# Performance work log

Measured on AMD Instinct MI355X. Metric: run time of the kernel, lower is better.

The kernel has to match this reference:

```python
import jax, jax.numpy as jnp
import numpy as np

HEADS = 8
NEG = -1e9
EPS = 1e-9


def setup_inputs() -> dict:
    key = jax.random.key(0)
    ks = jax.random.split(key, 24)
    N, D, E = 2048, 512, 64
    s = 0.02
    inp = {
        "xyz": jax.random.normal(ks[0], (N, 3), jnp.float32),
        "str_feat": jax.random.normal(ks[1], (N, D), jnp.float32),
        "esm_feat": jax.random.normal(ks[2], (N, E), jnp.float32),
        "y_hat": jax.random.uniform(ks[3], (N, 1), jnp.float32),
        "distance_mask": jax.random.randint(ks[4], (N, N), 0, 2, jnp.int32),
        "t": jnp.ones((1,), jnp.float32),
        "band_width": jnp.ones((1,), jnp.float32),
        "max_iter": 5,
        # main projections (torch Linear layout: y = x @ W.T + b)
        "Wq": jax.random.normal(ks[5], (D, D), jnp.float32) * s,
        "bq": jnp.zeros((D,), jnp.float32),
        "Wk": jax.random.normal(ks[6], (D, D), jnp.float32) * s,
        "bk": jnp.zeros((D,), jnp.float32),
        "Wv": jax.random.normal(ks[7], (D, D), jnp.float32) * s,
        "bv": jnp.zeros((D,), jnp.float32),
        "Wo": jax.random.normal(ks[8], (D, D), jnp.float32) * s,
        "bo": jnp.zeros((D,), jnp.float32),
        # esm projections (computed in the original forward but unused downstream)
        "Weq": jax.random.normal(ks[9], (E, E), jnp.float32) * s,
        "beq": jnp.zeros((E,), jnp.float32),
        "Wek": jax.random.normal(ks[10], (E, E), jnp.float32) * s,
        "bek": jnp.zeros((E,), jnp.float32),
        "Wev": jax.random.normal(ks[11], (E, E), jnp.float32) * s,
        "bev": jnp.zeros((E,), jnp.float32),
        "Weo": jax.random.normal(ks[12], (E, E), jnp.float32) * s,
        "beo": jnp.zeros((E,), jnp.float32),
    }
    return inp


def reference(xyz, str_feat, esm_feat, y_hat, distance_mask, t, band_width, max_iter,
              Wq, bq, Wk, bk, Wv, bv, Wo, bo,
              Weq, beq, Wek, bek, Wev, bev, Weo, beo):
    N, D = str_feat.shape
    h = HEADS
    dh = D // h

    q = str_feat @ Wq.T + bq
    k = str_feat @ Wk.T + bk
    v = str_feat @ Wv.T + bv
    # esm projections: computed in the original forward but never used (dead code; DCE'd under jit)
    _esm_q = esm_feat @ Weq.T + beq
    _esm_k = esm_feat @ Wek.T + bek
    _esm_v = esm_feat @ Wev.T + bev

    # [h, N, dh]
    qh = q.reshape(N, h, dh).transpose(1, 0, 2)
    kh = k.reshape(N, h, dh).transpose(1, 0, 2)
    vh = v.reshape(N, h, dh).transpose(1, 0, 2)

    scores = jnp.einsum('hnd,hmd->hnm', qh, kh) / jnp.sqrt(jnp.asarray(dh, qh.dtype))
    mask = (distance_mask > 0)[None]              # [1, N, N]
    yw = y_hat[:, 0][None, :]                     # [1, N] per-target weight
    inv_two_bw2 = 1.0 / (2.0 * band_width[0] ** 2)
    temp = t[0]

    def step(carry, _):
        xyz_c, _x = carry
        # squared pairwise distances via the expanded form (avoids [N,N,3])
        sq = jnp.sum(xyz_c * xyz_c, axis=-1)
        d2 = sq[:, None] + sq[None, :] - 2.0 * (xyz_c @ xyz_c.T)
        kern = jnp.exp(-d2 * inv_two_bw2)          # [N, N] band-width kernel
        logits = scores / temp + jnp.log(kern * yw + EPS)[None]
        logits = jnp.where(mask, logits, NEG)
        attn = jax.nn.softmax(logits, axis=-1)     # [h, N, N]
        xyz_new = jnp.einsum('nm,md->nd', attn.mean(0), xyz_c)  # mean-shift step
        x_new = jnp.einsum('hnm,hmd->hnd', attn, vh)            # [h, N, dh]
        return (xyz_new, x_new), None

    (xyz_out, xh), _ = jax.lax.scan(step, (xyz, jnp.zeros_like(vh)), None, length=max_iter)
    x = xh.transpose(1, 0, 2).reshape(N, D)
    out = x @ Wo.T + bo
    return xyz_out, out
```

## Files before the change

### kernel.cpp

```cpp
#include <hip/hip_runtime.h>


typedef __attribute__((ext_vector_type(8))) short bf16x8;
typedef __attribute__((ext_vector_type(4))) float f32x4;

__device__ __forceinline__ unsigned short f2bf(float f) {
    unsigned int u = __float_as_uint(f);
    u += 0x7fff + ((u >> 16) & 1);
    return (unsigned short)(u >> 16);
}
__device__ __forceinline__ float bf2f(unsigned short u) {
    return __uint_as_float((unsigned int)u << 16);
}

union EU { bf16x8 v; unsigned short u[8]; };

__global__ __launch_bounds__(256)
void conv_all(const float* __restrict__ strf,
              const float* __restrict__ Wq, const float* __restrict__ Wk,
              const float* __restrict__ Wv, const float* __restrict__ Wo,
              const int* __restrict__ dmask,
              unsigned short* __restrict__ sA, unsigned short* __restrict__ sW,
              unsigned char* __restrict__ mby)
{
    const long base = (long)(blockIdx.x * 256 + threadIdx.x) * 8;
    if (base >= 2097152) {
        const long rel = base - 2097152;
        int4 a = *reinterpret_cast<const int4*>(dmask + rel);
        int4 b = *reinterpret_cast<const int4*>(dmask + rel + 4);
        unsigned long long p = 0;
        p |= (a.x > 0) ? 0x01ULL : 0;  p |= (a.y > 0) ? 0x0100ULL : 0;
        p |= (a.z > 0) ? 0x010000ULL : 0;  p |= (a.w > 0) ? 0x01000000ULL : 0;
        p |= (b.x > 0) ? 0x0100000000ULL : 0;  p |= (b.y > 0) ? 0x010000000000ULL : 0;
        p |= (b.z > 0) ? 0x01000000000000ULL : 0;  p |= (b.w > 0) ? 0x0100000000000000ULL : 0;
        *reinterpret_cast<unsigned long long*>(mby + rel) = p;
        return;
    }
    const float* src;
    unsigned short* dst;
    if (base < 1048576) {
        src = strf + base; dst = sA + base;
    } else {
        const long rel = base - 1048576;
        const int seg = (int)(rel >> 18);
        const long off = rel & 262143;
        const float* Ws[4] = {Wq, Wk, Wv, Wo};
        src = Ws[seg] + off;
        dst = sW + (long)seg * 262144 + off;
    }
    float4 a = *reinterpret_cast<const float4*>(src);
    float4 b = *reinterpret_cast<const float4*>(src + 4);
    EU o;
    o.u[0] = f2bf(a.x); o.u[1] = f2bf(a.y); o.u[2] = f2bf(a.z); o.u[3] = f2bf(a.w);
    o.u[4] = f2bf(b.x); o.u[5] = f2bf(b.y); o.u[6] = f2bf(b.z); o.u[7] = f2bf(b.w);
    *reinterpret_cast<bf16x8*>(dst) = o.v;
}

__global__ __launch_bounds__(256)
void qkv_mfma(const unsigned short* __restrict__ sA,
              const unsigned short* __restrict__ sW,
              const float* __restrict__ bq, const float* __restrict__ bk,
              const float* __restrict__ bv,
              unsigned short* __restrict__ qh, unsigned short* __restrict__ kh,
              unsigned short* __restrict__ vT)
{
    const int z  = blockIdx.z;
    const int bx = blockIdx.x;
    const int by = blockIdx.y;
    const int tid = threadIdx.x;
    const int wv = tid >> 6;
    const int lane = tid & 63;
    const int row  = lane & 15;
    const int koct = (lane >> 4) * 8;
    const int n0 = bx * 64;

    const unsigned short* Ap = sA + (long)(n0 + wv * 16 + row) * 512;
    const unsigned short* Bp = sW + (long)z * 262144 + (long)(by * 64 + row) * 512;

    f32x4 acc[4] = {};
#pragma unroll
    for (int k0 = 0; k0 < 512; k0 += 32) {
        bf16x8 a = *reinterpret_cast<const bf16x8*>(Ap + k0 + koct);
#pragma unroll
        for (int t = 0; t < 4; t++) {
            bf16x8 b = *reinterpret_cast<const bf16x8*>(Bp + (long)(t * 16) * 512 + k0 + koct);
            acc[t] = __builtin_amdgcn_mfma_f32_16x16x32_bf16(a, b, acc[t], 0, 0, 0);
        }
    }

    if (z == 2) {
        const int rbase = n0 + wv * 16 + (lane >> 4) * 4;
#pragma unroll
        for (int t = 0; t < 4; t++) {
            const int d = by * 64 + t * 16 + (lane & 15);
            const float bb = bv[d];
            ushort4 o;
            o.x = f2bf(acc[t][0] + bb); o.y = f2bf(acc[t][1] + bb);
            o.z = f2bf(acc[t][2] + bb); o.w = f2bf(acc[t][3] + bb);
            *reinterpret_cast<ushort4*>(vT + (long)d * 2048 + rbase) = o;
        }
        return;
    }

    __shared__ float ls[64][68];
    const int lrb = wv * 16 + (lane >> 4) * 4;
    const int lcb = lane & 15;
#pragma unroll
    for (int t = 0; t < 4; t++)
#pragma unroll
        for (int r = 0; r < 4; r++)
            ls[lrb + r][t * 16 + lcb] = acc[t][r];
    __syncthreads();

    const float* bias = (z == 0) ? bq : bk;
    unsigned short* dst = (z == 0) ? qh : kh;
    const int r2 = tid >> 2;
    const int c2 = (tid & 3) * 16;
    float sv[16];
#pragma unroll
    for (int j = 0; j < 4; j++) {
        float4 s = *reinterpret_cast<const float4*>(&ls[r2][c2 + j * 4]);
        float4 bb = *reinterpret_cast<const float4*>(bias + by * 64 + c2 + j * 4);
        sv[j*4+0] = s.x + bb.x; sv[j*4+1] = s.y + bb.y;
        sv[j*4+2] = s.z + bb.z; sv[j*4+3] = s.w + bb.w;
    }
    EU o0, o1;
#pragma unroll
    for (int j = 0; j < 8; j++) { o0.u[j] = f2bf(sv[j]); o1.u[j] = f2bf(sv[8 + j]); }
    unsigned short* dp = dst + (long)(n0 + r2) * 512 + by * 64 + c2;
    *reinterpret_cast<bf16x8*>(dp)     = o0.v;
    *reinterpret_cast<bf16x8*>(dp + 8) = o1.v;
}

__global__ __launch_bounds__(256)
void scores_rows(const unsigned short* __restrict__ qh,
                 const unsigned short* __restrict__ kh,
                 const unsigned char* __restrict__ mby,
                 const float* __restrict__ tptr,
                 unsigned short* __restrict__ Ebf)
{
    const int h  = blockIdx.y;
    const int n0 = blockIdx.x * 16;
    const int tid = threadIdx.x;
    const int wv = tid >> 6;
    const int lane = tid & 63;
    const float scale = 1.0f / (8.0f * tptr[0]);

    __shared__ unsigned short lsb[4][16][260];

    const int arow = lane & 15;
    const int koct = (lane >> 4) * 8;
    const unsigned short* Aq = qh + (long)(n0 + arow) * 512 + h * 64;
    const bf16x8 aq0 = *reinterpret_cast<const bf16x8*>(Aq + koct);
    const bf16x8 aq1 = *reinterpret_cast<const bf16x8*>(Aq + 32 + koct);

    const int lr = (lane >> 4) * 4;
    const int lc = lane & 15;
    const int rlo = lane >> 5;
    const int cch = lane & 31;

#pragma unroll
    for (int half = 0; half < 2; half++) {
        const int mbase = wv * 512 + half * 256;
#pragma unroll
        for (int mt = 0; mt < 16; mt++) {
            const unsigned short* Bk = kh + (long)(mbase + mt * 16 + arow) * 512 + h * 64;
            bf16x8 b0 = *reinterpret_cast<const bf16x8*>(Bk + koct);
            bf16x8 b1 = *reinterpret_cast<const bf16x8*>(Bk + 32 + koct);
            f32x4 c = {};
            c = __builtin_amdgcn_mfma_f32_16x16x32_bf16(aq0, b0, c, 0, 0, 0);
            c = __builtin_amdgcn_mfma_f32_16x16x32_bf16(aq1, b1, c, 0, 0, 0);
#pragma unroll
            for (int r = 0; r < 4; r++)
                lsb[wv][lr + r][mt * 16 + lc] = f2bf(__expf(c[r] * scale));
        }
#pragma unroll
        for (int rp = 0; rp < 8; rp++) {
            const int row = rp * 2 + rlo;
            const int gn = n0 + row;
            const int m = mbase + cch * 8;
            EU e;
            e.v = *reinterpret_cast<const bf16x8*>(&lsb[wv][row][cch * 8]);
            unsigned long long mk =
                *reinterpret_cast<const unsigned long long*>(mby + (long)gn * 2048 + m);
            EU o;
#pragma unroll
            for (int j = 0; j < 8; j++)
                o.u[j] = ((mk >> (8 * j)) & 0xff) ? e.u[j] : (unsigned short)0;
            *reinterpret_cast<bf16x8*>(Ebf + ((long)h * 2048 + gn) * 2048 + m) = o.v;
        }
    }
}

__global__ __launch_bounds__(256)
void ms_iter(const unsigned short* __restrict__ Ebf,
             const float* __restrict__ xyz_src,
             float* __restrict__ xyz_dst,
             const float* __restrict__ y_hat,
             const float* __restrict__ bwp,
             unsigned short* __restrict__ gbf,
             float* __restrict__ invzb,
             int wlast)
{
    const int n = blockIdx.x;
    const int tid = threadIdx.x;
    const int lane = tid & 63;
    const int wave = tid >> 6;
    const int m0 = tid * 8;

    __shared__ unsigned short Es[8][4][512];
    __shared__ float red[64];

    {
        const unsigned short* gp = Ebf + (long)n * 2048 + wave * 512 + lane * 8;
#pragma unroll
        for (int h = 0; h < 8; h++) {
            __builtin_amdgcn_global_load_lds(
                (const __attribute__((address_space(1))) unsigned int*)(gp + (long)h * 4194304),
                (__attribute__((address_space(3))) unsigned int*)&Es[h][wave][0],
                16, 0, 0);
        }
    }

    const float bw = bwp[0];
    const float c2k = 1.0f / (2.0f * bw * bw);
    const float xn = xyz_src[n * 3 + 0];
    const float yn = xyz_src[n * 3 + 1];
    const float zn = xyz_src[n * 3 + 2];
    const float sqn = xn * xn + yn * yn + zn * zn;

    float mx[8], my[8], mz[8];
    {
        const float4* xp = reinterpret_cast<const float4*>(xyz_src + (long)m0 * 3);
        float4 a = xp[0], b = xp[1], c = xp[2], d = xp[3], e = xp[4], f = xp[5];
        mx[0]=a.x; my[0]=a.y; mz[0]=a.z;  mx[1]=a.w; my[1]=b.x; mz[1]=b.y;
        mx[2]=b.z; my[2]=b.w; mz[2]=c.x;  mx[3]=c.y; my[3]=c.z; mz[3]=c.w;
        mx[4]=d.x; my[4]=d.y; mz[4]=d.z;  mx[5]=d.w; my[5]=e.x; mz[5]=e.y;
        mx[6]=e.z; my[6]=e.w; mz[6]=f.x;  mx[7]=f.y; my[7]=f.z; mz[7]=f.w;
    }
    float4 yh0 = *reinterpret_cast<const float4*>(y_hat + m0);
    float4 yh1 = *reinterpret_cast<const float4*>(y_hat + m0 + 4);
    float yh[8] = {yh0.x, yh0.y, yh0.z, yh0.w, yh1.x, yh1.y, yh1.z, yh1.w};

    float g[8];
#pragma unroll
    for (int j = 0; j < 8; j++) {
        const float d2 = sqn + (mx[j]*mx[j] + my[j]*my[j] + mz[j]*mz[j])
                       - 2.0f * (xn*mx[j] + yn*my[j] + zn*mz[j]);
        g[j] = __expf(-d2 * c2k) * yh[j] + 1e-9f;
    }

    __syncthreads();

    EU E[8];
#pragma unroll
    for (int h = 0; h < 8; h++)
        E[h].v = *reinterpret_cast<const bf16x8*>(&Es[h][wave][lane * 8]);

    float z[8];
#pragma unroll
    for (int h = 0; h < 8; h++) {
        float zz = 0.f;
#pragma unroll
        for (int j = 0; j < 8; j++) zz += bf2f(E[h].u[j]) * g[j];
        z[h] = zz;
    }

#pragma unroll
    for (int h = 0; h < 8; h++) {
        float v = z[h];
#pragma unroll
        for (int off = 32; off > 0; off >>= 1) v += __shfl_down(v, off, 64);
        if (lane == 0) red[wave * 8 + h] = v;
    }
    __syncthreads();
    if (tid < 8) {
        const float s = red[tid] + red[8 + tid] + red[16 + tid] + red[24 + tid];
        const float iz = 1.0f / s;
        red[32 + tid] = iz;
        if (wlast) invzb[tid * 2048 + n] = iz;
    }
    __syncthreads();
    float invz[8];
#pragma unroll
    for (int h = 0; h < 8; h++) invz[h] = red[32 + h];

    float ax = 0.f, ay = 0.f, az = 0.f;
#pragma unroll
    for (int j = 0; j < 8; j++) {
        float w = 0.f;
#pragma unroll
        for (int h = 0; h < 8; h++) w += bf2f(E[h].u[j]) * invz[h];
        w *= 0.125f * g[j];
        ax += w * mx[j]; ay += w * my[j]; az += w * mz[j];
    }
    if (wlast) {
        EU og;
#pragma unroll
        for (int j = 0; j < 8; j++) og.u[j] = f2bf(g[j]);
        *reinterpret_cast<bf16x8*>(gbf + (long)n * 2048 + m0) = og.v;
    }

    float v3[3] = {ax, ay, az};
#pragma unroll
    for (int c = 0; c < 3; c++) {
        float v = v3[c];
#pragma unroll
        for (int off = 32; off > 0; off >>= 1) v += __shfl_down(v, off, 64);
        if (lane == 0) red[40 + c * 4 + wave] = v;
    }
    __syncthreads();
    if (tid < 3) {
        xyz_dst[n * 3 + tid] = red[40 + tid * 4 + 0] + red[40 + tid * 4 + 1] +
                               red[40 + tid * 4 + 2] + red[40 + tid * 4 + 3];
    }
}

__global__ __launch_bounds__(256)
void av_mfma(const unsigned short* __restrict__ Ebf,
             const unsigned short* __restrict__ gbf,
             const unsigned short* __restrict__ vT,
             float* __restrict__ P)
{
    const int h  = blockIdx.z;
    const int s  = blockIdx.y;
    const int bx = blockIdx.x;
    const int tid = threadIdx.x;
    const int wv = tid >> 6;
    const int lane = tid & 63;
    const int n0 = bx * 64;
    const int kc = s * 512;

    __shared__ unsigned short As[64][132];

    const int mrow = lane & 15;
    const int koct = (lane >> 4) * 8;
    const int srow = tid >> 4;
    const int skk  = (tid & 15) * 8;

    f32x4 acc[4] = {};
    for (int kt = 0; kt < 4; kt++) {
        const int kb = kc + kt * 128;
        __syncthreads();
#pragma unroll
        for (int l = 0; l < 4; l++) {
            const int row = l * 16 + srow;
            EU e, gg;
            e.v  = *reinterpret_cast<const bf16x8*>(Ebf + ((long)h * 2048 + n0 + row) * 2048 + kb + skk);
            gg.v = *reinterpret_cast<const bf16x8*>(gbf + (long)(n0 + row) * 2048 + kb + skk);
            EU a;
#pragma unroll
            for (int j = 0; j < 8; j++)
                a.u[j] = f2bf(bf2f(e.u[j]) * bf2f(gg.u[j]));
            *reinterpret_cast<bf16x8*>(&As[row][skk]) = a.v;
        }
        __syncthreads();
#pragma unroll
        for (int k2 = 0; k2 < 128; k2 += 32) {
            bf16x8 a = *reinterpret_cast<const bf16x8*>(&As[wv * 16 + mrow][k2 + koct]);
#pragma unroll
            for (int t = 0; t < 4; t++) {
                bf16x8 b = *reinterpret_cast<const bf16x8*>(
                    vT + ((long)h * 64 + t * 16 + mrow) * 2048 + kb + k2 + koct);
                acc[t] = __builtin_amdgcn_mfma_f32_16x16x32_bf16(a, b, acc[t], 0, 0, 0);
            }
        }
    }

    float* Pp = P + (long)s * 1048576;
    const int rbase = n0 + wv * 16 + (lane >> 4) * 4;
    const int dcol = lane & 15;
#pragma unroll
    for (int t = 0; t < 4; t++)
#pragma unroll
        for (int r = 0; r < 4; r++)
            Pp[(long)(rbase + r) * 512 + h * 64 + t * 16 + dcol] = acc[t][r];
}

__global__ __launch_bounds__(256)
void av_red(const float* __restrict__ P, const float* __restrict__ invzb,
            unsigned short* __restrict__ xc)
{
    const long idx = (long)(blockIdx.x * 256 + threadIdx.x) * 8;
    const int n = (int)(idx >> 9);
    const int d0 = (int)(idx & 511);
    const float iz = invzb[(d0 >> 6) * 2048 + n];
    float s[8] = {};
#pragma unroll
    for (int p = 0; p < 4; p++) {
        const float* pp = P + (long)p * 1048576 + idx;
        float4 a = *reinterpret_cast<const float4*>(pp);
        float4 b = *reinterpret_cast<const float4*>(pp + 4);
        s[0] += a.x; s[1] += a.y; s[2] += a.z; s[3] += a.w;
        s[4] += b.x; s[5] += b.y; s[6] += b.z; s[7] += b.w;
    }
    EU o;
#pragma unroll
    for (int j = 0; j < 8; j++) o.u[j] = f2bf(s[j] * iz);
    *reinterpret_cast<bf16x8*>(xc + idx) = o.v;
}

__global__ __launch_bounds__(256)
void out_mfma(const unsigned short* __restrict__ xc,
              const unsigned short* __restrict__ sW,
              const float* __restrict__ bo,
              float* __restrict__ out)
{
    const int bx = blockIdx.x;
    const int by = blockIdx.y;
    const int wv = threadIdx.x >> 6;
    const int lane = threadIdx.x & 63;
    const int row  = lane & 15;
    const int koct = (lane >> 4) * 8;
    const int n0 = bx * 64;

    const unsigned short* Ap = xc + (long)(n0 + wv * 16 + row) * 512;
    const unsigned short* Bp = sW + 3L * 262144 + (long)(by * 64 + row) * 512;

    f32x4 acc[4] = {};
#pragma unroll
    for (int k0 = 0; k0 < 512; k0 += 32) {
        bf16x8 a = *reinterpret_cast<const bf16x8*>(Ap + k0 + koct);
#pragma unroll
        for (int t = 0; t < 4; t++) {
            bf16x8 b = *reinterpret_cast<const bf16x8*>(Bp + (long)(t * 16) * 512 + k0 + koct);
            acc[t] = __builtin_amdgcn_mfma_f32_16x16x32_bf16(a, b, acc[t], 0, 0, 0);
        }
    }

    const int rbase = n0 + wv * 16 + (lane >> 4) * 4;
    const int dcol = lane & 15;
#pragma unroll
    for (int t = 0; t < 4; t++) {
        const int col = by * 64 + t * 16 + dcol;
        const float bb = bo[col];
#pragma unroll
        for (int r = 0; r < 4; r++)
            out[(long)(rbase + r) * 512 + col] = acc[t][r] + bb;
    }
}

extern "C" void kernel_launch(void* const* d_in, const int* in_sizes, int n_in,
                              void* d_out, int out_size, void* d_ws, size_t ws_size,
                              hipStream_t stream)
{
    (void)in_sizes; (void)n_in; (void)out_size; (void)ws_size;

    const float* xyz   = (const float*)d_in[0];
    const float* strf  = (const float*)d_in[1];
    const float* yhat  = (const float*)d_in[3];
    const int*   dmask = (const int*)d_in[4];
    const float* tptr  = (const float*)d_in[5];
    const float* bwptr = (const float*)d_in[6];
    const float* Wq = (const float*)d_in[8];
    const float* bq = (const float*)d_in[9];
    const float* Wk = (const float*)d_in[10];
    const float* bk = (const float*)d_in[11];
    const float* Wv = (const float*)d_in[12];
    const float* bv = (const float*)d_in[13];
    const float* Wo = (const float*)d_in[14];
    const float* bo = (const float*)d_in[15];
    float* outp = (float*)d_out;

    char* wsb = (char*)d_ws;
    float* Ppart         = (float*)(wsb);
    unsigned short* xc   = (unsigned short*)(wsb + (16L << 20));
    unsigned short* sA   = (unsigned short*)(wsb + (18L << 20));
    unsigned short* sW   = (unsigned short*)(wsb + (20L << 20));
    unsigned short* qh   = (unsigned short*)(wsb + (22L << 20));
    unsigned short* kh   = (unsigned short*)(wsb + (24L << 20));
    unsigned short* vT   = (unsigned short*)(wsb + (26L << 20));
    float* xyzA          = (float*)(wsb + (28L << 20));
    float* xyzB          = xyzA + 8192;
    unsigned char* mby   = (unsigned char*)(wsb + (30L << 20));
    unsigned short* Ebf  = (unsigned short*)(wsb + (34L << 20));
    unsigned short* gbf  = (unsigned short*)(wsb + (98L << 20));
    float* invzb         = (float*)(wsb + (106L << 20));

    dim3 blk(256, 1, 1);

    conv_all<<<dim3(3072), blk, 0, stream>>>(strf, Wq, Wk, Wv, Wo, dmask, sA, sW, mby);
    qkv_mfma<<<dim3(32, 8, 3), blk, 0, stream>>>(sA, sW, bq, bk, bv, qh, kh, vT);

    scores_rows<<<dim3(128, 8), blk, 0, stream>>>(qh, kh, mby, tptr, Ebf);

    const float* src = xyz;
    float* dsts[5] = {xyzA, xyzB, xyzA, xyzB, outp};
    for (int it = 0; it < 5; it++) {
        ms_iter<<<dim3(2048), blk, 0, stream>>>(Ebf, src, dsts[it], yhat, bwptr,
                                                gbf, invzb, it == 4 ? 1 : 0);
        src = dsts[it];
    }

    av_mfma<<<dim3(32, 4, 8), blk, 0, stream>>>(Ebf, gbf, vT, Ppart);
    av_red<<<dim3(512), blk, 0, stream>>>(Ppart, invzb, xc);
    out_mfma<<<dim3(32, 8), blk, 0, stream>>>(xc, sW, bo, outp + 6144);
}
```

Measured before the change: 318.6 us.

## Store masked scores row-major across heads and fuse split-K reduction into output GEMM

The masked exp-scores buffer moves from a head-major [h][n][m] layout to a row-major [n][h][m] layout. Each ms_iter block, which handles one row across all 8 heads, now reads one contiguous 32 KB region instead of 8 strided slices. The separate av_red kernel is removed: out_mfma now sums the four split-K partials, applies the normalizer and converts to bf16 inline. This saves a launch and an intermediate buffer round trip, but out_mfma now re-reads the fp32 partials once per output column block (8 times).

```diff
diff --git a/kernel.cpp b/kernel.cpp
--- a/kernel.cpp
+++ b/kernel.cpp
@@ -137,7 +137,7 @@
                  const unsigned short* __restrict__ kh,
                  const unsigned char* __restrict__ mby,
                  const float* __restrict__ tptr,
-                 unsigned short* __restrict__ Ebf)
+                 unsigned short* __restrict__ E2)
 {
     const int h  = blockIdx.y;
     const int n0 = blockIdx.x * 16;
@@ -187,13 +187,13 @@
 #pragma unroll
             for (int j = 0; j < 8; j++)
                 o.u[j] = ((mk >> (8 * j)) & 0xff) ? e.u[j] : (unsigned short)0;
-            *reinterpret_cast<bf16x8*>(Ebf + ((long)h * 2048 + gn) * 2048 + m) = o.v;
-        }
-    }
-}
-
-__global__ __launch_bounds__(256)
-void ms_iter(const unsigned short* __restrict__ Ebf,
+            *reinterpret_cast<bf16x8*>(E2 + (long)gn * 16384 + h * 2048 + m) = o.v;
+        }
+    }
+}
+
+__global__ __launch_bounds__(256)
+void ms_iter(const unsigned short* __restrict__ E2,
              const float* __restrict__ xyz_src,
              float* __restrict__ xyz_dst,
              const float* __restrict__ y_hat,
@@ -208,16 +208,16 @@
     const int wave = tid >> 6;
     const int m0 = tid * 8;
 
-    __shared__ unsigned short Es[8][4][512];
+    __shared__ unsigned short Es[16384];
     __shared__ float red[64];
 
     {
-        const unsigned short* gp = Ebf + (long)n * 2048 + wave * 512 + lane * 8;
-#pragma unroll
-        for (int h = 0; h < 8; h++) {
+        const unsigned short* gp = E2 + (long)n * 16384 + wave * 4096 + lane * 8;
+#pragma unroll
+        for (int c = 0; c < 8; c++) {
             __builtin_amdgcn_global_load_lds(
-                (const __attribute__((address_space(1))) unsigned int*)(gp + (long)h * 4194304),
-                (__attribute__((address_space(3))) unsigned int*)&Es[h][wave][0],
+                (const __attribute__((address_space(1))) unsigned int*)(gp + c * 512),
+                (__attribute__((address_space(3))) unsigned int*)&Es[wave * 4096 + c * 512],
                 16, 0, 0);
         }
     }
@@ -255,7 +255,7 @@
     EU E[8];
 #pragma unroll
     for (int h = 0; h < 8; h++)
-        E[h].v = *reinterpret_cast<const bf16x8*>(&Es[h][wave][lane * 8]);
+        E[h].v = *reinterpret_cast<const bf16x8*>(&Es[h * 2048 + m0]);
 
     float z[8];
 #pragma unroll
@@ -317,7 +317,7 @@
 }
 
 __global__ __launch_bounds__(256)
-void av_mfma(const unsigned short* __restrict__ Ebf,
+void av_mfma(const unsigned short* __restrict__ E2,
              const unsigned short* __restrict__ gbf,
              const unsigned short* __restrict__ vT,
              float* __restrict__ P)
@@ -346,7 +346,7 @@
         for (int l = 0; l < 4; l++) {
             const int row = l * 16 + srow;
             EU e, gg;
-            e.v  = *reinterpret_cast<const bf16x8*>(Ebf + ((long)h * 2048 + n0 + row) * 2048 + kb + skk);
+            e.v  = *reinterpret_cast<const bf16x8*>(E2 + (long)(n0 + row) * 16384 + h * 2048 + kb + skk);
             gg.v = *reinterpret_cast<const bf16x8*>(gbf + (long)(n0 + row) * 2048 + kb + skk);
             EU a;
 #pragma unroll
@@ -378,30 +378,8 @@
 }
 
 __global__ __launch_bounds__(256)
-void av_red(const float* __restrict__ P, const float* __restrict__ invzb,
-            unsigned short* __restrict__ xc)
-{
-    const long idx = (long)(blockIdx.x * 256 + threadIdx.x) * 8;
-    const int n = (int)(idx >> 9);
-    const int d0 = (int)(idx & 511);
-    const float iz = invzb[(d0 >> 6) * 2048 + n];
-    float s[8] = {};
-#pragma unroll
-    for (int p = 0; p < 4; p++) {
-        const float* pp = P + (long)p * 1048576 + idx;
-        float4 a = *reinterpret_cast<const float4*>(pp);
-        float4 b = *reinterpret_cast<const float4*>(pp + 4);
-        s[0] += a.x; s[1] += a.y; s[2] += a.z; s[3] += a.w;
-        s[4] += b.x; s[5] += b.y; s[6] += b.z; s[7] += b.w;
-    }
-    EU o;
-#pragma unroll
-    for (int j = 0; j < 8; j++) o.u[j] = f2bf(s[j] * iz);
-    *reinterpret_cast<bf16x8*>(xc + idx) = o.v;
-}
-
-__global__ __launch_bounds__(256)
-void out_mfma(const unsigned short* __restrict__ xc,
+void out_mfma(const float* __restrict__ P,
+              const float* __restrict__ invzb,
               const unsigned short* __restrict__ sW,
               const float* __restrict__ bo,
               float* __restrict__ out)
@@ -413,18 +391,31 @@
     const int row  = lane & 15;
     const int koct = (lane >> 4) * 8;
     const int n0 = bx * 64;
-
-    const unsigned short* Ap = xc + (long)(n0 + wv * 16 + row) * 512;
+    const int n  = n0 + wv * 16 + row;
+
     const unsigned short* Bp = sW + 3L * 262144 + (long)(by * 64 + row) * 512;
 
     f32x4 acc[4] = {};
 #pragma unroll
     for (int k0 = 0; k0 < 512; k0 += 32) {
-        bf16x8 a = *reinterpret_cast<const bf16x8*>(Ap + k0 + koct);
+        const int k = k0 + koct;
+        float s[8] = {};
+#pragma unroll
+        for (int p = 0; p < 4; p++) {
+            const float* pp = P + (long)p * 1048576 + (long)n * 512 + k;
+            float4 x = *reinterpret_cast<const float4*>(pp);
+            float4 y = *reinterpret_cast<const float4*>(pp + 4);
+            s[0] += x.x; s[1] += x.y; s[2] += x.z; s[3] += x.w;
+            s[4] += y.x; s[5] += y.y; s[6] += y.z; s[7] += y.w;
+        }
+        const float iz = invzb[(k >> 6) * 2048 + n];
+        EU a;
+#pragma unroll
+        for (int j = 0; j < 8; j++) a.u[j] = f2bf(s[j] * iz);
 #pragma unroll
         for (int t = 0; t < 4; t++) {
             bf16x8 b = *reinterpret_cast<const bf16x8*>(Bp + (long)(t * 16) * 512 + k0 + koct);
-            acc[t] = __builtin_amdgcn_mfma_f32_16x16x32_bf16(a, b, acc[t], 0, 0, 0);
+            acc[t] = __builtin_amdgcn_mfma_f32_16x16x32_bf16(a.v, b, acc[t], 0, 0, 0);
         }
     }
 
@@ -464,7 +455,6 @@
 
     char* wsb = (char*)d_ws;
     float* Ppart         = (float*)(wsb);
-    unsigned short* xc   = (unsigned short*)(wsb + (16L << 20));
     unsigned short* sA   = (unsigned short*)(wsb + (18L << 20));
     unsigned short* sW   = (unsigned short*)(wsb + (20L << 20));
     unsigned short* qh   = (unsigned short*)(wsb + (22L << 20));
@@ -473,7 +463,7 @@
     float* xyzA          = (float*)(wsb + (28L << 20));
     float* xyzB          = xyzA + 8192;
     unsigned char* mby   = (unsigned char*)(wsb + (30L << 20));
-    unsigned short* Ebf  = (unsigned short*)(wsb + (34L << 20));
+    unsigned short* E2   = (unsigned short*)(wsb + (34L << 20));
     unsigned short* gbf  = (unsigned short*)(wsb + (98L << 20));
     float* invzb         = (float*)(wsb + (106L << 20));
 
@@ -482,17 +472,16 @@
     conv_all<<<dim3(3072), blk, 0, stream>>>(strf, Wq, Wk, Wv, Wo, dmask, sA, sW, mby);
     qkv_mfma<<<dim3(32, 8, 3), blk, 0, stream>>>(sA, sW, bq, bk, bv, qh, kh, vT);
 
-    scores_rows<<<dim3(128, 8), blk, 0, stream>>>(qh, kh, mby, tptr, Ebf);
+    scores_rows<<<dim3(128, 8), blk, 0, stream>>>(qh, kh, mby, tptr, E2);
 
     const float* src = xyz;
     float* dsts[5] = {xyzA, xyzB, xyzA, xyzB, outp};
     for (int it = 0; it < 5; it++) {
-        ms_iter<<<dim3(2048), blk, 0, stream>>>(Ebf, src, dsts[it], yhat, bwptr,
+        ms_iter<<<dim3(2048), blk, 0, stream>>>(E2, src, dsts[it], yhat, bwptr,
                                                 gbf, invzb, it == 4 ? 1 : 0);
         src = dsts[it];
     }
 
-    av_mfma<<<dim3(32, 4, 8), blk, 0, stream>>>(Ebf, gbf, vT, Ppart);
-    av_red<<<dim3(512), blk, 0, stream>>>(Ppart, invzb, xc);
-    out_mfma<<<dim3(32, 8), blk, 0, stream>>>(xc, sW, bo, outp + 6144);
-}
+    av_mfma<<<dim3(32, 4, 8), blk, 0, stream>>>(E2, gbf, vT, Ppart);
+    out_mfma<<<dim3(32, 8), blk, 0, stream>>>(Ppart, invzb, sW, bo, outp + 6144);
+}
```

After: 323.2 us. About the same (+1.5%).
